# Optimization experiments

Hardware: AMD Instinct MI355X
Metric: run time of the kernel (lower is better)

Reference implementation:

```python
import jax, jax.numpy as jnp
import numpy as np

D_MODEL = 2048
D_KV = 512
D_Q = 1536
N_HEADS = 16
HEAD_DIM = 128
ROPE_BASE = 10000.0


def apply_rope(x, past_len=0):
    # x: [B, H, S, D]; interleaved-pair rotation (pairs (2i, 2i+1))
    B, H, S, D = x.shape
    half = D // 2
    pos = (jnp.arange(S) + past_len).astype(jnp.float32)
    inv_freq = 1.0 / (ROPE_BASE ** (jnp.arange(half, dtype=jnp.float32) * 2.0 / D))
    ang = pos[:, None] * inv_freq[None, :]          # [S, half]
    cos, sin = jnp.cos(ang), jnp.sin(ang)
    x1 = x[..., 0::2]
    x2 = x[..., 1::2]
    r1 = x1 * cos - x2 * sin
    r2 = x1 * sin + x2 * cos
    return jnp.stack([r1, r2], axis=-1).reshape(x.shape)


def setup_inputs() -> dict:
    key = jax.random.key(0)
    ks = jax.random.split(key, 16)
    s = 0.02
    inp = {
        "h": jax.random.normal(ks[0], (2, 2048, D_MODEL), dtype=jnp.float32),
        # weights stored [in, out] (y = x @ W + b)
        "W_DKV": jax.random.normal(ks[1], (D_MODEL, D_KV)) * s,
        "b_DKV": jnp.zeros((D_KV,)),
        "W_UK": jax.random.normal(ks[2], (D_KV, N_HEADS * HEAD_DIM)) * s,
        "b_UK": jnp.zeros((N_HEADS * HEAD_DIM,)),
        "W_UV": jax.random.normal(ks[3], (D_KV, N_HEADS * HEAD_DIM)) * s,
        "b_UV": jnp.zeros((N_HEADS * HEAD_DIM,)),
        "W_DQ": jax.random.normal(ks[4], (D_MODEL, D_Q)) * s,
        "b_DQ": jnp.zeros((D_Q,)),
        "W_UQ": jax.random.normal(ks[5], (D_Q, N_HEADS * HEAD_DIM)) * s,
        "b_UQ": jnp.zeros((N_HEADS * HEAD_DIM,)),
        "W_KR": jax.random.normal(ks[6], (D_MODEL, D_MODEL)) * s,
        "b_KR": jnp.zeros((D_MODEL,)),
        "W_O": jax.random.normal(ks[7], (D_MODEL, D_MODEL)) * s,
        "b_O": jnp.zeros((D_MODEL,)),
    }
    return inp


def reference(h, W_DKV, b_DKV, W_UK, b_UK, W_UV, b_UV, W_DQ, b_DQ,
              W_UQ, b_UQ, W_KR, b_KR, W_O, b_O):
    B, S, _ = h.shape

    def split_heads(x):  # [B,S,H*D] -> [B,H,S,D]
        return x.reshape(B, S, N_HEADS, HEAD_DIM).transpose(0, 2, 1, 3)

    # latent KV path (prefill: no cache)
    c_KV = h @ W_DKV + b_DKV                     # [B,S,d_kv] latent cache
    k_C = split_heads(c_KV @ W_UK + b_UK)        # [B,H,S,Dh]
    v_C = split_heads(c_KV @ W_UV + b_UV)        # [B,H,S,Dh]

    # decoupled RoPE K path
    kr_cache = h @ W_KR + b_KR                   # [B,S,d_model]
    k_R = apply_rope(split_heads(kr_cache))      # [B,H,S,Dh]
    k = jnp.concatenate([k_C, k_R], axis=-1)     # [B,H,S,2*Dh]

    # latent Q path
    c_Q = h @ W_DQ + b_DQ
    q_C = split_heads(c_Q @ W_UQ + b_UQ)
    q_R = apply_rope(q_C, past_len=0)
    q = jnp.concatenate([q_C, q_R], axis=-1)     # [B,H,S,2*Dh]

    # causal attention
    scale = 1.0 / jnp.sqrt(jnp.float32(q.shape[-1]))
    scores = jnp.einsum("bhqd,bhkd->bhqk", q, k) * scale
    causal = jnp.tril(jnp.ones((S, S), dtype=bool))
    scores = jnp.where(causal, scores, jnp.finfo(scores.dtype).min)
    attn = jax.nn.softmax(scores, axis=-1)
    ctx = jnp.einsum("bhqk,bhkd->bhqd", attn, v_C)
    ctx = ctx.transpose(0, 2, 1, 3).reshape(B, S, N_HEADS * HEAD_DIM)
    out = ctx @ W_O + b_O
    return (out, c_KV, kr_cache)
```

## Files before the change

### kernel.cpp

```cpp
#include <hip/hip_runtime.h>
#include <cstdint>
#include <cstddef>

typedef __bf16 bf16;
typedef __bf16 bf16x8 __attribute__((ext_vector_type(8)));
typedef float  f32x4  __attribute__((ext_vector_type(4)));

#define INVF_C 0.20762050593046014f

__device__ __forceinline__ void async_copy16(const void* g, void* l)
{
    auto gp = (__attribute__((address_space(1))) const void*)(reinterpret_cast<uintptr_t>(g));
    auto lp = (__attribute__((address_space(3))) void*)(uint32_t)(reinterpret_cast<uintptr_t>(l));
    __builtin_amdgcn_global_load_lds(gp, lp, 16, 0, 0);
}

__global__ void cast_to_bf16(const float* __restrict__ in, bf16* __restrict__ out, int n)
{
    const int i = (blockIdx.x * 256 + threadIdx.x) * 4;
    if (i < n) {
        const float4 v = *(const float4*)(in + i);
        out[i]     = (bf16)v.x;
        out[i + 1] = (bf16)v.y;
        out[i + 2] = (bf16)v.z;
        out[i + 3] = (bf16)v.w;
    }
}

__global__ void transpose_cast(const float* __restrict__ in, bf16* __restrict__ out,
                               int R, int Ccols)
{
    __shared__ float tile[32][33];
    const int c0 = blockIdx.x * 32;
    const int r0 = blockIdx.y * 32;
    const int tx = threadIdx.x, ty = threadIdx.y;
    for (int i = ty; i < 32; i += 8)
        tile[i][tx] = in[(size_t)(r0 + i) * Ccols + c0 + tx];
    __syncthreads();
    for (int i = ty; i < 32; i += 8)
        out[(size_t)(c0 + i) * R + r0 + tx] = (bf16)tile[tx][i];
}

__device__ __forceinline__ void gemm_core(const bf16* __restrict__ A,
                                          const bf16* __restrict__ Bt,
                                          int K, int m0, int n0,
                                          bf16* As, bf16* Bs,
                                          f32x4 (&acc)[4][4])
{
    const int tid  = threadIdx.x;
    const int wave = tid >> 6;
    const int lane = tid & 63;
    const int quad = lane >> 4;
    const int l15  = lane & 15;
    const int wm   = (wave >> 1) * 64;
    const int wn   = (wave & 1) * 64;

    const int srow = lane >> 3;
    const int scol = (lane & 7) * 8;
    const bf16* Ab = A  + (size_t)(m0 + wave * 32 + srow) * K + scol;
    const bf16* Bb = Bt + (size_t)(n0 + wave * 32 + srow) * K + scol;
    bf16* AsW = &As[(wave * 32) * 64];
    bf16* BsW = &Bs[(wave * 32) * 64];

    for (int k0 = 0; k0 < K; k0 += 64) {
        __syncthreads();
#pragma unroll
        for (int i = 0; i < 4; ++i) {
            async_copy16(Ab + (size_t)(i * 8) * K + k0, AsW + i * 8 * 64);
            async_copy16(Bb + (size_t)(i * 8) * K + k0, BsW + i * 8 * 64);
        }
        __syncthreads();
#pragma unroll
        for (int ks = 0; ks < 2; ++ks) {
            bf16x8 af[4], bfr[4];
#pragma unroll
            for (int i = 0; i < 4; ++i)
                af[i] = *(const bf16x8*)&As[(wm + i * 16 + l15) * 64 + ks * 32 + quad * 8];
#pragma unroll
            for (int j = 0; j < 4; ++j)
                bfr[j] = *(const bf16x8*)&Bs[(wn + j * 16 + l15) * 64 + ks * 32 + quad * 8];
#pragma unroll
            for (int i = 0; i < 4; ++i)
#pragma unroll
                for (int j = 0; j < 4; ++j)
                    acc[i][j] = __builtin_amdgcn_mfma_f32_16x16x32_bf16(af[i], bfr[j], acc[i][j], 0, 0, 0);
        }
    }
}

__global__ __launch_bounds__(256, 2)
void gemm_bt(const bf16* __restrict__ A, const bf16* __restrict__ Bt,
             const float* __restrict__ bias, float* __restrict__ C,
             bf16* __restrict__ Cb, int M, int N, int K)
{
    __shared__ bf16 As[128 * 64];
    __shared__ bf16 Bs[128 * 64];
    const int m0 = blockIdx.y * 128;
    const int n0 = blockIdx.x * 128;
    f32x4 acc[4][4] = {};
    gemm_core(A, Bt, K, m0, n0, As, Bs, acc);

    const int tid  = threadIdx.x;
    const int wave = tid >> 6;
    const int lane = tid & 63;
    const int quad = lane >> 4;
    const int l15  = lane & 15;
    const int wm   = (wave >> 1) * 64;
    const int wn   = (wave & 1) * 64;

#pragma unroll
    for (int j = 0; j < 4; ++j) {
        const int col = n0 + wn + j * 16 + l15;
        const float bv = bias[col];
#pragma unroll
        for (int i = 0; i < 4; ++i) {
            const int row = m0 + wm + i * 16 + quad * 4;
#pragma unroll
            for (int r = 0; r < 4; ++r) {
                const float v = acc[i][j][r] + bv;
                if (C)  C [(size_t)(row + r) * N + col] = v;
                if (Cb) Cb[(size_t)(row + r) * N + col] = (bf16)v;
            }
        }
    }
}

__global__ __launch_bounds__(256, 2)
void gemm_batch1(const bf16* __restrict__ A, const bf16* __restrict__ WtAll,
                 const float* __restrict__ bDKV, const float* __restrict__ bKR,
                 const float* __restrict__ bDQ,
                 float* __restrict__ cKV_f, bf16* __restrict__ cKVb,
                 float* __restrict__ krc_f, bf16* __restrict__ cQ)
{
    __shared__ bf16 As[128 * 64];
    __shared__ bf16 Bs[128 * 64];
    const int m0 = blockIdx.y * 128;
    const int n0 = blockIdx.x * 128;
    f32x4 acc[4][4] = {};
    gemm_core(A, WtAll, 2048, m0, n0, As, Bs, acc);

    const int tid  = threadIdx.x;
    const int wave = tid >> 6;
    const int lane = tid & 63;
    const int quad = lane >> 4;
    const int l15  = lane & 15;
    const int wm   = (wave >> 1) * 64;
    const int wn   = (wave & 1) * 64;

    if (n0 < 512) {
#pragma unroll
        for (int j = 0; j < 4; ++j) {
            const int col = n0 + wn + j * 16 + l15;
            const float bv = bDKV[col];
#pragma unroll
            for (int i = 0; i < 4; ++i) {
                const int row = m0 + wm + i * 16 + quad * 4;
#pragma unroll
                for (int r = 0; r < 4; ++r) {
                    const float v = acc[i][j][r] + bv;
                    cKV_f[(size_t)(row + r) * 512 + col] = v;
                    cKVb [(size_t)(row + r) * 512 + col] = (bf16)v;
                }
            }
        }
    } else if (n0 < 2560) {
#pragma unroll
        for (int j = 0; j < 4; ++j) {
            const int col = n0 + wn + j * 16 + l15;
            const int cl  = col - 512;
            const float bv = bKR[cl];
#pragma unroll
            for (int i = 0; i < 4; ++i) {
                const int row = m0 + wm + i * 16 + quad * 4;
#pragma unroll
                for (int r = 0; r < 4; ++r)
                    krc_f[(size_t)(row + r) * 2048 + cl] = acc[i][j][r] + bv;
            }
        }
    } else {
#pragma unroll
        for (int j = 0; j < 4; ++j) {
            const int col = n0 + wn + j * 16 + l15;
            const int cl  = col - 2560;
            const float bv = bDQ[cl];
#pragma unroll
            for (int i = 0; i < 4; ++i) {
                const int row = m0 + wm + i * 16 + quad * 4;
#pragma unroll
                for (int r = 0; r < 4; ++r)
                    cQ[(size_t)(row + r) * 1536 + cl] = (bf16)(acc[i][j][r] + bv);
            }
        }
    }
}

__global__ __launch_bounds__(256, 2)
void gemm_batch45(const bf16* __restrict__ A, const bf16* __restrict__ Wt45,
                  const float* __restrict__ bUK, const float* __restrict__ bUV,
                  bf16* __restrict__ kC, bf16* __restrict__ vC)
{
    __shared__ bf16 As[128 * 64];
    __shared__ bf16 Bs[128 * 64];
    const int m0 = blockIdx.y * 128;
    const int n0 = blockIdx.x * 128;
    f32x4 acc[4][4] = {};
    gemm_core(A, Wt45, 512, m0, n0, As, Bs, acc);

    const int tid  = threadIdx.x;
    const int wave = tid >> 6;
    const int lane = tid & 63;
    const int quad = lane >> 4;
    const int l15  = lane & 15;
    const int wm   = (wave >> 1) * 64;
    const int wn   = (wave & 1) * 64;

    const bool isK = (n0 < 2048);
    bf16* outp = isK ? kC : vC;
    const float* bp = isK ? bUK : bUV;
    const int base = isK ? 0 : 2048;
#pragma unroll
    for (int j = 0; j < 4; ++j) {
        const int col = n0 + wn + j * 16 + l15;
        const int cl  = col - base;
        const float bv = bp[cl];
#pragma unroll
        for (int i = 0; i < 4; ++i) {
            const int row = m0 + wm + i * 16 + quad * 4;
#pragma unroll
            for (int r = 0; r < 4; ++r)
                outp[(size_t)(row + r) * 2048 + cl] = (bf16)(acc[i][j][r] + bv);
        }
    }
}

__global__ __launch_bounds__(256, 2)
void gemm_q_rope(const bf16* __restrict__ A, const bf16* __restrict__ Bt,
                 const float* __restrict__ bias,
                 bf16* __restrict__ qC, bf16* __restrict__ qR)
{
    __shared__ bf16 As[128 * 64];
    __shared__ bf16 Bs[128 * 64];
    const int m0 = blockIdx.y * 128;
    const int n0 = blockIdx.x * 128;
    f32x4 acc[4][4] = {};
    gemm_core(A, Bt, 1536, m0, n0, As, Bs, acc);

    const int tid  = threadIdx.x;
    const int wave = tid >> 6;
    const int lane = tid & 63;
    const int quad = lane >> 4;
    const int l15  = lane & 15;
    const int wm   = (wave >> 1) * 64;
    const int wn   = (wave & 1) * 64;
    const int odd  = l15 & 1;

#pragma unroll
    for (int j = 0; j < 4; ++j) {
        const int col = n0 + wn + j * 16 + l15;
        const float bv = bias[col];
        const float freq = exp2f(-(float)((col & 127) >> 1) * INVF_C);
#pragma unroll
        for (int i = 0; i < 4; ++i) {
            const int rowb = m0 + wm + i * 16 + quad * 4;
#pragma unroll
            for (int r = 0; r < 4; ++r) {
                const int row = rowb + r;
                const float v = acc[i][j][r] + bv;
                qC[(size_t)row * 2048 + col] = (bf16)v;
                const float vp = __shfl_xor(v, 1, 64);
                const float x1 = odd ? vp : v;
                const float x2 = odd ? v  : vp;
                const float ang = (float)(row & 2047) * freq;
                float sn, cs;
                __sincosf(ang, &sn, &cs);
                qR[(size_t)row * 2048 + col] =
                    (bf16)(odd ? (x1 * sn + x2 * cs) : (x1 * cs - x2 * sn));
            }
        }
    }
}

__global__ void transpose_v(const bf16* __restrict__ vC, bf16* __restrict__ vT)
{
    __shared__ bf16 tile[32][33];
    const int bh = blockIdx.z, b = bh >> 4, h = bh & 15;
    const int s0 = blockIdx.x * 32, d0 = blockIdx.y * 32;
    const int tx = threadIdx.x, ty = threadIdx.y;
    for (int i = ty; i < 32; i += 8)
        tile[i][tx] = vC[((size_t)(b * 2048 + s0 + i)) * 2048 + h * 128 + d0 + tx];
    __syncthreads();
    for (int i = ty; i < 32; i += 8)
        vT[((size_t)(bh * 128 + d0 + i)) * 2048 + s0 + tx] = tile[tx][i];
}

__global__ void rope_heads_f(const float* __restrict__ in, bf16* __restrict__ out)
{
    const int idx = blockIdx.x * 256 + threadIdx.x;
    const int j = idx & 63;
    const int h = (idx >> 6) & 15;
    const int s = (idx >> 10) & 2047;
    const int b = idx >> 21;
    const size_t src = ((size_t)(b * 2048 + s)) * 2048 + h * 128 + 2 * j;
    const float x1 = in[src], x2 = in[src + 1];
    const float ang = (float)s * exp2f(-(float)j * INVF_C);
    float sn, cs;
    __sincosf(ang, &sn, &cs);
    out[src]     = (bf16)(x1 * cs - x2 * sn);
    out[src + 1] = (bf16)(x1 * sn + x2 * cs);
}

__global__ __launch_bounds__(512, 2)
void mla_attn(const bf16* __restrict__ qCp, const bf16* __restrict__ qRp,
              const bf16* __restrict__ kCp, const bf16* __restrict__ kRp,
              const bf16* __restrict__ Vt, bf16* __restrict__ ctx)
{
    __shared__ bf16 Ks[64 * 264];
    __shared__ bf16 Vs[128 * 72];
    __shared__ bf16 Ps[128 * 72];
    const int bh   = blockIdx.x;
    const int b    = bh >> 4, hh = bh & 15;
    const int yq   = blockIdx.y;
    const int qt   = (yq < 8) ? (2 * yq) : (31 - 2 * yq);
    const int q0   = qt * 128;
    const int tid  = threadIdx.x;
    const int wave = tid >> 6;
    const int lane = tid & 63;
    const int quad = lane >> 4;
    const int l15  = lane & 15;
    const int wq   = q0 + wave * 16;

    bf16x8 qf[8];
    {
        const size_t qoff = ((size_t)(b * 2048 + wq + l15)) * 2048
                          + hh * 128 + quad * 8;
#pragma unroll
        for (int ks = 0; ks < 4; ++ks) {
            qf[ks]     = *(const bf16x8*)(qCp + qoff + ks * 32);
            qf[4 + ks] = *(const bf16x8*)(qRp + qoff + ks * 32);
        }
    }

    float mstate[4], lstate[4];
    f32x4 o[8];
#pragma unroll
    for (int r = 0; r < 4; ++r) { mstate[r] = -1e30f; lstate[r] = 0.0f; }
#pragma unroll
    for (int dt = 0; dt < 8; ++dt) { f32x4 z = {0.f, 0.f, 0.f, 0.f}; o[dt] = z; }

    const int krow = tid >> 4, kcol = (tid & 15) * 8;
    const int vsr  = tid >> 3, vsc  = (tid & 7) * 8;

    bf16x8 stKC[2], stKR[2], stV[2];

    const int ntiles = 2 * qt + 2;

    {
#pragma unroll
        for (int it = 0; it < 2; ++it) {
            const int row = it * 32 + krow;
            const size_t g = ((size_t)(b * 2048 + row)) * 2048 + hh * 128 + kcol;
            stKC[it] = *(const bf16x8*)(kCp + g);
            stKR[it] = *(const bf16x8*)(kRp + g);
        }
#pragma unroll
        for (int it = 0; it < 2; ++it) {
            const int d = it * 64 + vsr;
            stV[it] = *(const bf16x8*)(Vt + ((size_t)(bh * 128 + d)) * 2048 + vsc);
        }
#pragma unroll
        for (int it = 0; it < 2; ++it) {
            const int row = it * 32 + krow;
            *(bf16x8*)&Ks[row * 264 + kcol]       = stKC[it];
            *(bf16x8*)&Ks[row * 264 + 128 + kcol] = stKR[it];
        }
#pragma unroll
        for (int it = 0; it < 2; ++it) {
            const int d = it * 64 + vsr;
            *(bf16x8*)&Vs[d * 72 + vsc] = stV[it];
        }
    }
    __syncthreads();

    for (int t = 0; t < ntiles; ++t) {
        const int kk0 = t * 64;

        if (t + 1 < ntiles) {
            const int nk0 = kk0 + 64;
#pragma unroll
            for (int it = 0; it < 2; ++it) {
                const int row = it * 32 + krow;
                const size_t g = ((size_t)(b * 2048 + nk0 + row)) * 2048 + hh * 128 + kcol;
                stKC[it] = *(const bf16x8*)(kCp + g);
                stKR[it] = *(const bf16x8*)(kRp + g);
            }
#pragma unroll
            for (int it = 0; it < 2; ++it) {
                const int d = it * 64 + vsr;
                stV[it] = *(const bf16x8*)(Vt + ((size_t)(bh * 128 + d)) * 2048 + nk0 + vsc);
            }
        }

        if (kk0 <= wq + 15) {
            f32x4 sc[4] = {};
#pragma unroll
            for (int ks = 0; ks < 8; ++ks)
#pragma unroll
                for (int j = 0; j < 4; ++j) {
                    bf16x8 kf = *(const bf16x8*)&Ks[(j * 16 + l15) * 264 + ks * 32 + quad * 8];
                    sc[j] = __builtin_amdgcn_mfma_f32_16x16x32_bf16(qf[ks], kf, sc[j], 0, 0, 0);
                }

            const bool diag = (kk0 + 63 > wq);
            float rowmax[4] = {-1e30f, -1e30f, -1e30f, -1e30f};
#pragma unroll
            for (int j = 0; j < 4; ++j) {
                const int kkcol = kk0 + j * 16 + l15;
#pragma unroll
                for (int r = 0; r < 4; ++r) {
                    float s = sc[j][r] * 0.0625f;
                    if (diag && (kkcol > wq + quad * 4 + r)) s = -1e30f;
                    sc[j][r] = s;
                    rowmax[r] = fmaxf(rowmax[r], s);
                }
            }
#pragma unroll
            for (int r = 0; r < 4; ++r) {
                float v = rowmax[r];
                v = fmaxf(v, __shfl_xor(v, 1, 64));
                v = fmaxf(v, __shfl_xor(v, 2, 64));
                v = fmaxf(v, __shfl_xor(v, 4, 64));
                v = fmaxf(v, __shfl_xor(v, 8, 64));
                rowmax[r] = v;
            }
            float alpha[4];
#pragma unroll
            for (int r = 0; r < 4; ++r) {
                const float mnew = fmaxf(mstate[r], rowmax[r]);
                alpha[r] = __expf(mstate[r] - mnew);
                mstate[r] = mnew;
            }
            float rowsum[4] = {0.f, 0.f, 0.f, 0.f};
#pragma unroll
            for (int j = 0; j < 4; ++j)
#pragma unroll
                for (int r = 0; r < 4; ++r) {
                    const float p = __expf(sc[j][r] - mstate[r]);
                    sc[j][r] = p;
                    rowsum[r] += p;
                }
#pragma unroll
            for (int r = 0; r < 4; ++r) {
                float v = rowsum[r];
                v += __shfl_xor(v, 1, 64);
                v += __shfl_xor(v, 2, 64);
                v += __shfl_xor(v, 4, 64);
                v += __shfl_xor(v, 8, 64);
                lstate[r] = lstate[r] * alpha[r] + v;
            }
#pragma unroll
            for (int j = 0; j < 4; ++j)
#pragma unroll
                for (int r = 0; r < 4; ++r)
                    Ps[(wave * 16 + quad * 4 + r) * 72 + j * 16 + l15] = (bf16)sc[j][r];
#pragma unroll
            for (int dt = 0; dt < 8; ++dt)
#pragma unroll
                for (int r = 0; r < 4; ++r)
                    o[dt][r] *= alpha[r];
#pragma unroll
            for (int ks2 = 0; ks2 < 2; ++ks2) {
                bf16x8 pf = *(const bf16x8*)&Ps[(wave * 16 + l15) * 72 + ks2 * 32 + quad * 8];
#pragma unroll
                for (int dt = 0; dt < 8; ++dt) {
                    bf16x8 vf = *(const bf16x8*)&Vs[(dt * 16 + l15) * 72 + ks2 * 32 + quad * 8];
                    o[dt] = __builtin_amdgcn_mfma_f32_16x16x32_bf16(pf, vf, o[dt], 0, 0, 0);
                }
            }
        }

        __syncthreads();
        if (t + 1 < ntiles) {
#pragma unroll
            for (int it = 0; it < 2; ++it) {
                const int row = it * 32 + krow;
                *(bf16x8*)&Ks[row * 264 + kcol]       = stKC[it];
                *(bf16x8*)&Ks[row * 264 + 128 + kcol] = stKR[it];
            }
#pragma unroll
            for (int it = 0; it < 2; ++it) {
                const int d = it * 64 + vsr;
                *(bf16x8*)&Vs[d * 72 + vsc] = stV[it];
            }
        }
        __syncthreads();
    }

    float inv_l[4];
#pragma unroll
    for (int r = 0; r < 4; ++r) inv_l[r] = 1.0f / lstate[r];
#pragma unroll
    for (int dt = 0; dt < 8; ++dt) {
        const int d = dt * 16 + l15;
#pragma unroll
        for (int r = 0; r < 4; ++r) {
            const int q = wq + quad * 4 + r;
            ctx[((size_t)(b * 2048 + q)) * 2048 + hh * 128 + d] = (bf16)(o[dt][r] * inv_l[r]);
        }
    }
}

extern "C" void kernel_launch(void* const* d_in, const int* in_sizes, int n_in,
                              void* d_out, int out_size, void* d_ws, size_t ws_size,
                              hipStream_t stream)
{
    const float* h     = (const float*)d_in[0];
    const float* W_DKV = (const float*)d_in[1];
    const float* b_DKV = (const float*)d_in[2];
    const float* W_UK  = (const float*)d_in[3];
    const float* b_UK  = (const float*)d_in[4];
    const float* W_UV  = (const float*)d_in[5];
    const float* b_UV  = (const float*)d_in[6];
    const float* W_DQ  = (const float*)d_in[7];
    const float* b_DQ  = (const float*)d_in[8];
    const float* W_UQ  = (const float*)d_in[9];
    const float* b_UQ  = (const float*)d_in[10];
    const float* W_KR  = (const float*)d_in[11];
    const float* b_KR  = (const float*)d_in[12];
    const float* W_O   = (const float*)d_in[13];
    const float* b_O   = (const float*)d_in[14];

    float* out   = (float*)d_out;
    float* cKV_f = out + (size_t)8388608;
    float* krc_f = out + (size_t)10485760;

    bf16* qC = (bf16*)d_out;
    bf16* qR = (bf16*)d_out + 8388608;

    bf16* ws    = (bf16*)d_ws;
    bf16* hb    = ws + 0;
    bf16* cKVb  = ws + 8388608;
    bf16* cQ    = ws + 10485760;
    bf16* WtAll = ws + 16777216;
    bf16* kC    = ws + 25165824;
    bf16* vC    = ws + 33554432;
    bf16* kR    = hb;
    bf16* vT    = WtAll;
    bf16* ctx   = vC;

    dim3 tb(32, 8);

    cast_to_bf16<<<8192, 256, 0, stream>>>(h, hb, 8388608);

    transpose_cast<<<dim3(16, 64), tb, 0, stream>>>(W_DKV, WtAll,           2048, 512);
    transpose_cast<<<dim3(64, 64), tb, 0, stream>>>(W_KR,  WtAll + 1048576, 2048, 2048);
    transpose_cast<<<dim3(48, 64), tb, 0, stream>>>(W_DQ,  WtAll + 5242880, 2048, 1536);

    gemm_batch1<<<dim3(32, 32), 256, 0, stream>>>(hb, WtAll, b_DKV, b_KR, b_DQ,
                                                  cKV_f, cKVb, krc_f, cQ);
    rope_heads_f<<<16384, 256, 0, stream>>>(krc_f, kR);

    transpose_cast<<<dim3(64, 16), tb, 0, stream>>>(W_UK, WtAll,           512, 2048);
    transpose_cast<<<dim3(64, 16), tb, 0, stream>>>(W_UV, WtAll + 1048576, 512, 2048);
    gemm_batch45<<<dim3(32, 32), 256, 0, stream>>>(cKVb, WtAll, b_UK, b_UV, kC, vC);

    transpose_cast<<<dim3(64, 48), tb, 0, stream>>>(W_UQ, WtAll, 1536, 2048);
    gemm_q_rope<<<dim3(16, 32), 256, 0, stream>>>(cQ, WtAll, b_UQ, qC, qR);

    transpose_v<<<dim3(64, 4, 32), tb, 0, stream>>>(vC, vT);

    mla_attn<<<dim3(32, 16), 512, 0, stream>>>(qC, qR, kC, kR, vT, ctx);

    transpose_cast<<<dim3(64, 64), tb, 0, stream>>>(W_O, WtAll, 2048, 2048);
    gemm_bt<<<dim3(16, 32), 256, 0, stream>>>(ctx, WtAll, b_O, out, nullptr, 4096, 2048, 2048);
}
```

Baseline: 535.6 us.

## Fuse K RoPE and V transpose into GEMM epilogues, merge weight transposes

Applies RoPE to the K projection directly in the first batched GEMM epilogue using lane shuffles, removing the separate rope kernel and its reread of the fp32 kr_cache. The K/V up-projection GEMM now writes V already transposed per head, which removes the transpose_v kernel. The three down-projection weight transposes are merged into one launch, and so are the two up-projection ones, and the workspace buffers are reassigned to fit. The V epilogue's transposed 4-element stores are strided in memory, and the added sincos work makes the GEMM epilogue heavier.

```diff
diff --git a/kernel.cpp b/kernel.cpp
--- a/kernel.cpp
+++ b/kernel.cpp
@@ -3,6 +3,7 @@
 #include <cstddef>
 
 typedef __bf16 bf16;
+typedef __bf16 bf16x4 __attribute__((ext_vector_type(4)));
 typedef __bf16 bf16x8 __attribute__((ext_vector_type(8)));
 typedef float  f32x4  __attribute__((ext_vector_type(4)));
 
@@ -41,6 +42,43 @@
         out[(size_t)(c0 + i) * R + r0 + tx] = (bf16)tile[tx][i];
 }
 
+__global__ void transpose_cast3(const float* __restrict__ w0,
+                                const float* __restrict__ w1,
+                                const float* __restrict__ w2,
+                                bf16* __restrict__ outAll)
+{
+    __shared__ float tile[32][33];
+    const int cg0 = blockIdx.x * 32;
+    const int r0  = blockIdx.y * 32;
+    const float* in; int cl0, Cc;
+    if (cg0 < 512)       { in = w0; cl0 = cg0;        Cc = 512;  }
+    else if (cg0 < 2560) { in = w1; cl0 = cg0 - 512;  Cc = 2048; }
+    else                 { in = w2; cl0 = cg0 - 2560; Cc = 1536; }
+    const int tx = threadIdx.x, ty = threadIdx.y;
+    for (int i = ty; i < 32; i += 8)
+        tile[i][tx] = in[(size_t)(r0 + i) * Cc + cl0 + tx];
+    __syncthreads();
+    for (int i = ty; i < 32; i += 8)
+        outAll[(size_t)(cg0 + i) * 2048 + r0 + tx] = (bf16)tile[tx][i];
+}
+
+__global__ void transpose_cast2(const float* __restrict__ w0,
+                                const float* __restrict__ w1,
+                                bf16* __restrict__ outAll)
+{
+    __shared__ float tile[32][33];
+    const int cg0 = blockIdx.x * 32;
+    const int r0  = blockIdx.y * 32;
+    const float* in = (cg0 < 2048) ? w0 : w1;
+    const int cl0 = cg0 & 2047;
+    const int tx = threadIdx.x, ty = threadIdx.y;
+    for (int i = ty; i < 32; i += 8)
+        tile[i][tx] = in[(size_t)(r0 + i) * 2048 + cl0 + tx];
+    __syncthreads();
+    for (int i = ty; i < 32; i += 8)
+        outAll[(size_t)(cg0 + i) * 512 + r0 + tx] = (bf16)tile[tx][i];
+}
+
 __device__ __forceinline__ void gemm_core(const bf16* __restrict__ A,
                                           const bf16* __restrict__ Bt,
                                           int K, int m0, int n0,
@@ -130,7 +168,8 @@
                  const float* __restrict__ bDKV, const float* __restrict__ bKR,
                  const float* __restrict__ bDQ,
                  float* __restrict__ cKV_f, bf16* __restrict__ cKVb,
-                 float* __restrict__ krc_f, bf16* __restrict__ cQ)
+                 float* __restrict__ krc_f, bf16* __restrict__ kR,
+                 bf16* __restrict__ cQ)
 {
     __shared__ bf16 As[128 * 64];
     __shared__ bf16 Bs[128 * 64];
@@ -164,17 +203,30 @@
             }
         }
     } else if (n0 < 2560) {
+        const int odd = l15 & 1;
 #pragma unroll
         for (int j = 0; j < 4; ++j) {
             const int col = n0 + wn + j * 16 + l15;
             const int cl  = col - 512;
             const float bv = bKR[cl];
+            const float freq = exp2f(-(float)((cl & 127) >> 1) * INVF_C);
 #pragma unroll
             for (int i = 0; i < 4; ++i) {
-                const int row = m0 + wm + i * 16 + quad * 4;
-#pragma unroll
-                for (int r = 0; r < 4; ++r)
-                    krc_f[(size_t)(row + r) * 2048 + cl] = acc[i][j][r] + bv;
+                const int rowb = m0 + wm + i * 16 + quad * 4;
+#pragma unroll
+                for (int r = 0; r < 4; ++r) {
+                    const int row = rowb + r;
+                    const float v = acc[i][j][r] + bv;
+                    krc_f[(size_t)row * 2048 + cl] = v;
+                    const float vp = __shfl_xor(v, 1, 64);
+                    const float x1 = odd ? vp : v;
+                    const float x2 = odd ? v  : vp;
+                    const float ang = (float)(row & 2047) * freq;
+                    float sn, cs;
+                    __sincosf(ang, &sn, &cs);
+                    kR[(size_t)row * 2048 + cl] =
+                        (bf16)(odd ? (x1 * sn + x2 * cs) : (x1 * cs - x2 * sn));
+                }
             }
         }
     } else {
@@ -197,7 +249,7 @@
 __global__ __launch_bounds__(256, 2)
 void gemm_batch45(const bf16* __restrict__ A, const bf16* __restrict__ Wt45,
                   const float* __restrict__ bUK, const float* __restrict__ bUV,
-                  bf16* __restrict__ kC, bf16* __restrict__ vC)
+                  bf16* __restrict__ kC, bf16* __restrict__ vT)
 {
     __shared__ bf16 As[128 * 64];
     __shared__ bf16 Bs[128 * 64];
@@ -214,21 +266,33 @@
     const int wm   = (wave >> 1) * 64;
     const int wn   = (wave & 1) * 64;
 
-    const bool isK = (n0 < 2048);
-    bf16* outp = isK ? kC : vC;
-    const float* bp = isK ? bUK : bUV;
-    const int base = isK ? 0 : 2048;
-#pragma unroll
-    for (int j = 0; j < 4; ++j) {
-        const int col = n0 + wn + j * 16 + l15;
-        const int cl  = col - base;
-        const float bv = bp[cl];
-#pragma unroll
-        for (int i = 0; i < 4; ++i) {
-            const int row = m0 + wm + i * 16 + quad * 4;
-#pragma unroll
-            for (int r = 0; r < 4; ++r)
-                outp[(size_t)(row + r) * 2048 + cl] = (bf16)(acc[i][j][r] + bv);
+    if (n0 < 2048) {
+#pragma unroll
+        for (int j = 0; j < 4; ++j) {
+            const int col = n0 + wn + j * 16 + l15;
+            const float bv = bUK[col];
+#pragma unroll
+            for (int i = 0; i < 4; ++i) {
+                const int row = m0 + wm + i * 16 + quad * 4;
+#pragma unroll
+                for (int r = 0; r < 4; ++r)
+                    kC[(size_t)(row + r) * 2048 + col] = (bf16)(acc[i][j][r] + bv);
+            }
+        }
+    } else {
+#pragma unroll
+        for (int j = 0; j < 4; ++j) {
+            const int cl = n0 + wn + j * 16 + l15 - 2048;
+            const int hloc = cl >> 7, d = cl & 127;
+            const float bv = bUV[cl];
+#pragma unroll
+            for (int i = 0; i < 4; ++i) {
+                const int rowb = m0 + wm + i * 16 + quad * 4;
+                const int bb = rowb >> 11, s = rowb & 2047;
+                bf16x4 p = { (bf16)(acc[i][j][0] + bv), (bf16)(acc[i][j][1] + bv),
+                             (bf16)(acc[i][j][2] + bv), (bf16)(acc[i][j][3] + bv) };
+                *(bf16x4*)(vT + ((size_t)((bb * 16 + hloc) * 128 + d)) * 2048 + s) = p;
+            }
         }
     }
 }
@@ -278,35 +342,6 @@
             }
         }
     }
-}
-
-__global__ void transpose_v(const bf16* __restrict__ vC, bf16* __restrict__ vT)
-{
-    __shared__ bf16 tile[32][33];
-    const int bh = blockIdx.z, b = bh >> 4, h = bh & 15;
-    const int s0 = blockIdx.x * 32, d0 = blockIdx.y * 32;
-    const int tx = threadIdx.x, ty = threadIdx.y;
-    for (int i = ty; i < 32; i += 8)
-        tile[i][tx] = vC[((size_t)(b * 2048 + s0 + i)) * 2048 + h * 128 + d0 + tx];
-    __syncthreads();
-    for (int i = ty; i < 32; i += 8)
-        vT[((size_t)(bh * 128 + d0 + i)) * 2048 + s0 + tx] = tile[tx][i];
-}
-
-__global__ void rope_heads_f(const float* __restrict__ in, bf16* __restrict__ out)
-{
-    const int idx = blockIdx.x * 256 + threadIdx.x;
-    const int j = idx & 63;
-    const int h = (idx >> 6) & 15;
-    const int s = (idx >> 10) & 2047;
-    const int b = idx >> 21;
-    const size_t src = ((size_t)(b * 2048 + s)) * 2048 + h * 128 + 2 * j;
-    const float x1 = in[src], x2 = in[src + 1];
-    const float ang = (float)s * exp2f(-(float)j * INVF_C);
-    float sn, cs;
-    __sincosf(ang, &sn, &cs);
-    out[src]     = (bf16)(x1 * cs - x2 * sn);
-    out[src + 1] = (bf16)(x1 * sn + x2 * cs);
 }
 
 __global__ __launch_bounds__(512, 2)
@@ -541,33 +576,26 @@
     bf16* cKVb  = ws + 8388608;
     bf16* cQ    = ws + 10485760;
     bf16* WtAll = ws + 16777216;
-    bf16* kC    = ws + 25165824;
-    bf16* vC    = ws + 33554432;
-    bf16* kR    = hb;
-    bf16* vT    = WtAll;
-    bf16* ctx   = vC;
+    bf16* kR    = ws + 25165824;
+    bf16* kC    = ws + 33554432;
+    bf16* vT    = hb;
+    bf16* ctx   = ws + 8388608;
 
     dim3 tb(32, 8);
 
     cast_to_bf16<<<8192, 256, 0, stream>>>(h, hb, 8388608);
 
-    transpose_cast<<<dim3(16, 64), tb, 0, stream>>>(W_DKV, WtAll,           2048, 512);
-    transpose_cast<<<dim3(64, 64), tb, 0, stream>>>(W_KR,  WtAll + 1048576, 2048, 2048);
-    transpose_cast<<<dim3(48, 64), tb, 0, stream>>>(W_DQ,  WtAll + 5242880, 2048, 1536);
+    transpose_cast3<<<dim3(128, 64), tb, 0, stream>>>(W_DKV, W_KR, W_DQ, WtAll);
 
     gemm_batch1<<<dim3(32, 32), 256, 0, stream>>>(hb, WtAll, b_DKV, b_KR, b_DQ,
-                                                  cKV_f, cKVb, krc_f, cQ);
-    rope_heads_f<<<16384, 256, 0, stream>>>(krc_f, kR);
-
-    transpose_cast<<<dim3(64, 16), tb, 0, stream>>>(W_UK, WtAll,           512, 2048);
-    transpose_cast<<<dim3(64, 16), tb, 0, stream>>>(W_UV, WtAll + 1048576, 512, 2048);
-    gemm_batch45<<<dim3(32, 32), 256, 0, stream>>>(cKVb, WtAll, b_UK, b_UV, kC, vC);
+                                                  cKV_f, cKVb, krc_f, kR, cQ);
+
+    transpose_cast2<<<dim3(128, 16), tb, 0, stream>>>(W_UK, W_UV, WtAll);
+    gemm_batch45<<<dim3(32, 32), 256, 0, stream>>>(cKVb, WtAll, b_UK, b_UV, kC, vT);
 
     transpose_cast<<<dim3(64, 48), tb, 0, stream>>>(W_UQ, WtAll, 1536, 2048);
     gemm_q_rope<<<dim3(16, 32), 256, 0, stream>>>(cQ, WtAll, b_UQ, qC, qR);
 
-    transpose_v<<<dim3(64, 4, 32), tb, 0, stream>>>(vC, vT);
-
     mla_attn<<<dim3(32, 16), 512, 0, stream>>>(qC, qR, kC, kR, vT, ctx);
 
     transpose_cast<<<dim3(64, 64), tb, 0, stream>>>(W_O, WtAll, 2048, 2048);
```

Result: no change. 538.5 us (+0.5%).
